# Kernel optimization log

Measured on AMD Instinct MI355X. Metric: run time of the kernel, lower is better.

## Reference

```python
import jax, jax.numpy as jnp
import numpy as np

B, C, H, W, P = 16, 512, 64, 64, 32


def setup_inputs() -> dict:
    key = jax.random.key(0)
    k1, k2, k3 = jax.random.split(key, 3)
    inputs = jax.random.normal(k1, (B, C, H, W), dtype=jnp.float32)
    weight = jax.random.uniform(k2, (P, C, 1, 1), dtype=jnp.float32)
    smooth_factor = jax.random.normal(k3, (P,), dtype=jnp.float32)
    return {"inputs": inputs, "weight": weight, "smooth_factor": smooth_factor}


def reference(inputs, weight, smooth_factor):
    b, c, h, w = inputs.shape
    p = weight.shape[0]
    n = h * w
    centers = weight.reshape(p, c)                      # [P,C]
    x = inputs.reshape(b, c, n)                         # [B,C,N]

    # distance-based logits: 2<c,x> - |x|^2 - |c|^2, clamped at 0
    cx = jnp.einsum('pc,bcn->bpn', centers, x)          # [B,P,N]
    x_sq = jnp.sum(x * x, axis=1, keepdims=True)        # [B,1,N]
    c_sq = jnp.sum(centers * centers, axis=1)[None, :, None]  # [1,P,1]
    beta = jax.nn.sigmoid(smooth_factor)                # [P]
    logits = jnp.minimum(2.0 * cx - x_sq - c_sq, 0.0) / beta[None, :, None]
    assign = jax.nn.softmax(logits, axis=1)             # [B,P,N]

    # assignment-weighted pooling
    qx = jnp.einsum('bpn,bcn->bpc', assign, x)          # [B,P,C]
    sum_ass = jnp.clip(jnp.sum(assign, axis=2, keepdims=True), 1e-5)  # [B,P,1]
    sigma = jnp.sqrt(beta / 2.0)                        # [P]
    out = (qx / sum_ass - centers[None, :, :]) / sigma[None, :, None]

    # L2-normalize over channel dim (torch F.normalize, eps=1e-12)
    norm = jnp.sqrt(jnp.sum(out * out, axis=2, keepdims=True))
    outputs = out / jnp.maximum(norm, 1e-12)
    outputs_t = jnp.transpose(outputs, (0, 2, 1))       # [B,C,P]
    assign_map = assign.reshape(b, p, h, w)             # [B,P,H,W]
    return outputs_t, assign_map
```

## Files before the change

### kernel.cpp

```cpp
#include <hip/hip_runtime.h>

constexpr int BB = 16;
constexpr int CC = 512;
constexpr int PP = 32;
constexpr int NN = 4096;

using f32x4 = __attribute__((ext_vector_type(4))) float;
using bf16x8 = __attribute__((ext_vector_type(8))) short;
typedef unsigned int uint;

__device__ __forceinline__ ushort f2bf(float f) {
  unsigned u = __builtin_bit_cast(unsigned, f);
  u += 0x7FFFu + ((u >> 16) & 1u);
  return (ushort)(u >> 16);
}

__global__ __launch_bounds__(64) void prep_kernel(
    const float* __restrict__ w, const float* __restrict__ sf,
    float* __restrict__ beta, float* __restrict__ rbeta,
    float* __restrict__ csq, float* __restrict__ sum_ass,
    ushort* __restrict__ chi, ushort* __restrict__ clo) {
  int p = blockIdx.x;
  int t = threadIdx.x;
  if (t < 16) sum_ass[p * 16 + t] = 0.f;
  float s = 0.f;
  int c8 = t * 8;
  float4 v0 = *(const float4*)&w[p * CC + c8];
  float4 v1 = *(const float4*)&w[p * CC + c8 + 4];
  ushort h[8], l[8];
  float vv[8] = {v0.x, v0.y, v0.z, v0.w, v1.x, v1.y, v1.z, v1.w};
#pragma unroll
  for (int i = 0; i < 8; ++i) {
    s = fmaf(vv[i], vv[i], s);
    h[i] = f2bf(vv[i]);
    float hf = __builtin_bit_cast(float, (uint)h[i] << 16);
    l[i] = f2bf(vv[i] - hf);
  }
  *(ushort4*)&chi[p * CC + c8] = make_ushort4(h[0], h[1], h[2], h[3]);
  *(ushort4*)&chi[p * CC + c8 + 4] = make_ushort4(h[4], h[5], h[6], h[7]);
  *(ushort4*)&clo[p * CC + c8] = make_ushort4(l[0], l[1], l[2], l[3]);
  *(ushort4*)&clo[p * CC + c8 + 4] = make_ushort4(l[4], l[5], l[6], l[7]);
#pragma unroll
  for (int off = 32; off; off >>= 1) s += __shfl_down(s, off);
  if (t == 0) {
    csq[p] = s;
    float e = __expf(-sf[p]);
    rbeta[p] = 1.f + e;
    beta[p] = 1.f / (1.f + e);
  }
}

__global__ __launch_bounds__(256) void assign_kernel(
    const float* __restrict__ x, const ushort* __restrict__ chi,
    const ushort* __restrict__ clo, const float* __restrict__ rbeta_,
    const float* __restrict__ csq_, float* __restrict__ assign_out,
    float* __restrict__ sum_ass) {
  int tid = threadIdx.x;
  int wv = tid >> 6, lane = tid & 63;
  int l15 = lane & 15, lg = lane >> 4;
  int b = blockIdx.x >> 5;
  int n0 = (blockIdx.x & 31) * 128 + wv * 32;

  const float* xb = x + (size_t)b * CC * NN + n0 + l15;

  f32x4 acc[2][2];
#pragma unroll
  for (int i = 0; i < 2; ++i)
#pragma unroll
    for (int j = 0; j < 2; ++j) acc[i][j] = {0.f, 0.f, 0.f, 0.f};
  float xsq[2] = {0.f, 0.f};

#pragma unroll 4
  for (int ks = 0; ks < 16; ++ks) {
    int c0 = ks * 32 + lg * 8;
    bf16x8 Ah0 = *(const bf16x8*)&chi[l15 * CC + c0];
    bf16x8 Ah1 = *(const bf16x8*)&chi[(l15 + 16) * CC + c0];
    bf16x8 Al0 = *(const bf16x8*)&clo[l15 * CC + c0];
    bf16x8 Al1 = *(const bf16x8*)&clo[(l15 + 16) * CC + c0];
#pragma unroll
    for (int nf = 0; nf < 2; ++nf) {
      float xv[8];
#pragma unroll
      for (int j = 0; j < 8; ++j)
        xv[j] = xb[(size_t)(c0 + j) * NN + nf * 16];
      union { bf16x8 v; ushort e[8]; } Bh, Bl;
#pragma unroll
      for (int j = 0; j < 8; ++j) {
        xsq[nf] = fmaf(xv[j], xv[j], xsq[nf]);
        ushort h = f2bf(xv[j]);
        float hf = __builtin_bit_cast(float, (uint)h << 16);
        Bh.e[j] = h;
        Bl.e[j] = f2bf(xv[j] - hf);
      }
      acc[0][nf] = __builtin_amdgcn_mfma_f32_16x16x32_bf16(Ah0, Bh.v, acc[0][nf], 0, 0, 0);
      acc[1][nf] = __builtin_amdgcn_mfma_f32_16x16x32_bf16(Ah1, Bh.v, acc[1][nf], 0, 0, 0);
      acc[0][nf] = __builtin_amdgcn_mfma_f32_16x16x32_bf16(Ah0, Bl.v, acc[0][nf], 0, 0, 0);
      acc[1][nf] = __builtin_amdgcn_mfma_f32_16x16x32_bf16(Ah1, Bl.v, acc[1][nf], 0, 0, 0);
      acc[0][nf] = __builtin_amdgcn_mfma_f32_16x16x32_bf16(Al0, Bh.v, acc[0][nf], 0, 0, 0);
      acc[1][nf] = __builtin_amdgcn_mfma_f32_16x16x32_bf16(Al1, Bh.v, acc[1][nf], 0, 0, 0);
    }
  }

#pragma unroll
  for (int nf = 0; nf < 2; ++nf) {
    xsq[nf] += __shfl_xor(xsq[nf], 16);
    xsq[nf] += __shfl_xor(xsq[nf], 32);
  }

  float csqv[2][4], rbv[2][4];
#pragma unroll
  for (int pf = 0; pf < 2; ++pf)
#pragma unroll
    for (int i = 0; i < 4; ++i) {
      int p = pf * 16 + lg * 4 + i;
      csqv[pf][i] = csq_[p];
      rbv[pf][i] = rbeta_[p];
    }

  float L[2][2][4];
  float m[2] = {-3.4e38f, -3.4e38f};
#pragma unroll
  for (int pf = 0; pf < 2; ++pf)
#pragma unroll
    for (int nf = 0; nf < 2; ++nf)
#pragma unroll
      for (int i = 0; i < 4; ++i) {
        float l = fminf(2.f * acc[pf][nf][i] - xsq[nf] - csqv[pf][i], 0.f) * rbv[pf][i];
        L[pf][nf][i] = l;
        m[nf] = fmaxf(m[nf], l);
      }
#pragma unroll
  for (int nf = 0; nf < 2; ++nf) {
    m[nf] = fmaxf(m[nf], __shfl_xor(m[nf], 16));
    m[nf] = fmaxf(m[nf], __shfl_xor(m[nf], 32));
  }
  float s[2] = {0.f, 0.f};
#pragma unroll
  for (int pf = 0; pf < 2; ++pf)
#pragma unroll
    for (int nf = 0; nf < 2; ++nf)
#pragma unroll
      for (int i = 0; i < 4; ++i) {
        float e = __expf(L[pf][nf][i] - m[nf]);
        L[pf][nf][i] = e;
        s[nf] += e;
      }
#pragma unroll
  for (int nf = 0; nf < 2; ++nf) {
    s[nf] += __shfl_xor(s[nf], 16);
    s[nf] += __shfl_xor(s[nf], 32);
    s[nf] = 1.f / s[nf];
  }

  float* aoB = assign_out + (size_t)b * PP * NN + n0 + l15;
#pragma unroll
  for (int pf = 0; pf < 2; ++pf)
#pragma unroll
    for (int i = 0; i < 4; ++i) {
      int p = pf * 16 + lg * 4 + i;
      float a0 = L[pf][0][i] * s[0];
      float a1 = L[pf][1][i] * s[1];
      aoB[(size_t)p * NN] = a0;
      aoB[(size_t)p * NN + 16] = a1;
      float v = a0 + a1;
      v += __shfl_xor(v, 1); v += __shfl_xor(v, 2);
      v += __shfl_xor(v, 4); v += __shfl_xor(v, 8);
      if (l15 == 0) atomicAdd(&sum_ass[b * PP + p], v);
    }
}

__global__ __launch_bounds__(256) void qx_kernel(
    const float* __restrict__ x, const float* __restrict__ assign,
    float* __restrict__ qx_part) {
  __shared__ ushort xbf[128][136];
  __shared__ ushort abf[32][136];

  int tid = threadIdx.x;
  int b = blockIdx.y;
  int kc = blockIdx.x >> 2;
  int ct = blockIdx.x & 3;
  int wv = tid >> 6, lane = tid & 63;
  int l15 = lane & 15, lg = lane >> 4;

  const float* xb = x + ((size_t)b * CC + ct * 128) * NN + kc * 512;
  const float* ab = assign + (size_t)b * PP * NN + kc * 512;

  int c_s = tid >> 1;
  int nh  = (tid & 1) << 6;
  int p_s = tid >> 3;
  int na  = (tid & 7) << 4;

  f32x4 acc[2][2];
#pragma unroll
  for (int i = 0; i < 2; ++i)
#pragma unroll
    for (int j = 0; j < 2; ++j) acc[i][j] = {0.f, 0.f, 0.f, 0.f};

  for (int ch = 0; ch < 4; ++ch) {
    int nb = ch * 128;
    if (ch) __syncthreads();
#pragma unroll
    for (int h = 0; h < 2; ++h) {
      float4 v[8];
#pragma unroll
      for (int i = 0; i < 8; ++i)
        v[i] = *(const float4*)&xb[(size_t)c_s * NN + nb + nh + h * 32 + i * 4];
#pragma unroll
      for (int i = 0; i < 8; ++i) {
        ushort4 u;
        u.x = f2bf(v[i].x); u.y = f2bf(v[i].y);
        u.z = f2bf(v[i].z); u.w = f2bf(v[i].w);
        *(ushort4*)&xbf[c_s][nh + h * 32 + i * 4] = u;
      }
    }
    {
      float4 v[4];
#pragma unroll
      for (int i = 0; i < 4; ++i)
        v[i] = *(const float4*)&ab[(size_t)p_s * NN + nb + na + i * 4];
#pragma unroll
      for (int i = 0; i < 4; ++i) {
        ushort4 u;
        u.x = f2bf(v[i].x); u.y = f2bf(v[i].y);
        u.z = f2bf(v[i].z); u.w = f2bf(v[i].w);
        *(ushort4*)&abf[p_s][na + i * 4] = u;
      }
    }
    __syncthreads();
#pragma unroll
    for (int ks = 0; ks < 4; ++ks) {
      int nf = ks * 32 + lg * 8;
      bf16x8 a0 = *(const bf16x8*)&abf[l15][nf];
      bf16x8 a1 = *(const bf16x8*)&abf[16 + l15][nf];
      bf16x8 b0 = *(const bf16x8*)&xbf[wv * 32 + l15][nf];
      bf16x8 b1 = *(const bf16x8*)&xbf[wv * 32 + 16 + l15][nf];
      acc[0][0] = __builtin_amdgcn_mfma_f32_16x16x32_bf16(a0, b0, acc[0][0], 0, 0, 0);
      acc[0][1] = __builtin_amdgcn_mfma_f32_16x16x32_bf16(a0, b1, acc[0][1], 0, 0, 0);
      acc[1][0] = __builtin_amdgcn_mfma_f32_16x16x32_bf16(a1, b0, acc[1][0], 0, 0, 0);
      acc[1][1] = __builtin_amdgcn_mfma_f32_16x16x32_bf16(a1, b1, acc[1][1], 0, 0, 0);
    }
  }

#pragma unroll
  for (int pf = 0; pf < 2; ++pf)
#pragma unroll
    for (int cf = 0; cf < 2; ++cf)
#pragma unroll
      for (int i = 0; i < 4; ++i) {
        int p = pf * 16 + lg * 4 + i;
        int c = ct * 128 + wv * 32 + cf * 16 + l15;
        qx_part[(((size_t)kc * BB + b) * PP + p) * CC + c] = acc[pf][cf][i];
      }
}

__global__ __launch_bounds__(256) void finalize_kernel(
    const float* __restrict__ qx_part, const float* __restrict__ w,
    const float* __restrict__ beta, const float* __restrict__ sum_ass,
    float* __restrict__ out_t) {
  int b = blockIdx.x >> 5;
  int p = blockIdx.x & 31;
  int tid = threadIdx.x;
  int wave = tid >> 6, lane = tid & 63;

  float inv_sa = 1.f / fmaxf(sum_ass[b * PP + p], 1e-5f);
  float rsig = rsqrtf(0.5f * beta[p]);

  int c0 = tid, c1 = tid + 256;
  float q0 = 0.f, q1 = 0.f;
#pragma unroll
  for (int kc = 0; kc < 8; ++kc) {
    const float* row = qx_part + (((size_t)kc * BB + b) * PP + p) * CC;
    q0 += row[c0];
    q1 += row[c1];
  }
  const float* wrow = w + (size_t)p * CC;
  float t0 = (q0 * inv_sa - wrow[c0]) * rsig;
  float t1 = (q1 * inv_sa - wrow[c1]) * rsig;

  float nr = t0 * t0 + t1 * t1;
#pragma unroll
  for (int off = 32; off; off >>= 1) nr += __shfl_down(nr, off);
  __shared__ float red[4];
  if (lane == 0) red[wave] = nr;
  __syncthreads();
  float norm2 = red[0] + red[1] + red[2] + red[3];
  float scale = 1.f / fmaxf(sqrtf(norm2), 1e-12f);

  float* ob = out_t + (size_t)b * CC * PP + p;
  ob[(size_t)c0 * PP] = t0 * scale;
  ob[(size_t)c1 * PP] = t1 * scale;
}

extern "C" void kernel_launch(void* const* d_in, const int* in_sizes, int n_in,
                              void* d_out, int out_size, void* d_ws,
                              size_t ws_size, hipStream_t stream) {
  const float* x = (const float*)d_in[0];
  const float* w = (const float*)d_in[1];
  const float* sf = (const float*)d_in[2];

  float* out_t = (float*)d_out;
  float* assign = out_t + (size_t)BB * CC * PP;

  float* ws = (float*)d_ws;
  float* beta = ws;
  float* rbeta = ws + 32;
  float* csq = ws + 64;
  float* sum_ass = ws + 96;
  float* qx_part = ws + 608;
  ushort* chi = (ushort*)(ws + 608 + 2097152);
  ushort* clo = chi + PP * CC;

  prep_kernel<<<PP, 64, 0, stream>>>(w, sf, beta, rbeta, csq, sum_ass,
                                     chi, clo);
  assign_kernel<<<512, 256, 0, stream>>>(x, chi, clo, rbeta, csq, assign,
                                         sum_ass);
  qx_kernel<<<dim3(32, BB), 256, 0, stream>>>(x, assign, qx_part);
  finalize_kernel<<<BB * PP, 256, 0, stream>>>(qx_part, w, beta, sum_ass,
                                               out_t);
}
```

Baseline: 85.66 us.

## Drop LDS staging in qx kernel, write bf16 assign, and atomically accumulate qx

The assign kernel now gives each wave 16 columns instead of 32, doubling the grid, and also writes a bf16 copy of the assignments for the second GEMM. The qx kernel drops shared-memory staging: each wave loads bf16 assign and fp32 x straight from global memory, converts x to bf16 in registers, and accumulates its partial result into qx with atomics. This removes the fp32 partial buffer and the reduction loop in finalize, and prep now zeroes the combined sum_ass and qx region. In exchange it adds many float atomics and relies on uncoalesced per-lane global loads without LDS reuse.

New measurement: 125.0 us. 1.46x slower.

```diff
diff --git a/kernel.cpp b/kernel.cpp
--- a/kernel.cpp
+++ b/kernel.cpp
@@ -18,11 +18,14 @@
 __global__ __launch_bounds__(64) void prep_kernel(
     const float* __restrict__ w, const float* __restrict__ sf,
     float* __restrict__ beta, float* __restrict__ rbeta,
-    float* __restrict__ csq, float* __restrict__ sum_ass,
+    float* __restrict__ csq, float* __restrict__ zbase,
     ushort* __restrict__ chi, ushort* __restrict__ clo) {
+  int t = threadIdx.x;
+  float4* z4 = (float4*)zbase;
+  for (int i = blockIdx.x * 64 + t; i < 65664; i += 32 * 64)
+    z4[i] = make_float4(0.f, 0.f, 0.f, 0.f);
+
   int p = blockIdx.x;
-  int t = threadIdx.x;
-  if (t < 16) sum_ass[p * 16 + t] = 0.f;
   float s = 0.f;
   int c8 = t * 8;
   float4 v0 = *(const float4*)&w[p * CC + c8];
@@ -50,25 +53,23 @@
   }
 }
 
-__global__ __launch_bounds__(256) void assign_kernel(
+__global__ __launch_bounds__(256, 4) void assign_kernel(
     const float* __restrict__ x, const ushort* __restrict__ chi,
     const ushort* __restrict__ clo, const float* __restrict__ rbeta_,
     const float* __restrict__ csq_, float* __restrict__ assign_out,
-    float* __restrict__ sum_ass) {
+    ushort* __restrict__ abf16, float* __restrict__ sum_ass) {
   int tid = threadIdx.x;
   int wv = tid >> 6, lane = tid & 63;
   int l15 = lane & 15, lg = lane >> 4;
-  int b = blockIdx.x >> 5;
-  int n0 = (blockIdx.x & 31) * 128 + wv * 32;
+  int b = blockIdx.x >> 6;
+  int n0 = (blockIdx.x & 63) * 64 + wv * 16;
 
   const float* xb = x + (size_t)b * CC * NN + n0 + l15;
 
-  f32x4 acc[2][2];
-#pragma unroll
-  for (int i = 0; i < 2; ++i)
-#pragma unroll
-    for (int j = 0; j < 2; ++j) acc[i][j] = {0.f, 0.f, 0.f, 0.f};
-  float xsq[2] = {0.f, 0.f};
+  f32x4 acc[2];
+  acc[0] = {0.f, 0.f, 0.f, 0.f};
+  acc[1] = {0.f, 0.f, 0.f, 0.f};
+  float xsq = 0.f;
 
 #pragma unroll 4
   for (int ks = 0; ks < 16; ++ks) {
@@ -77,35 +78,28 @@
     bf16x8 Ah1 = *(const bf16x8*)&chi[(l15 + 16) * CC + c0];
     bf16x8 Al0 = *(const bf16x8*)&clo[l15 * CC + c0];
     bf16x8 Al1 = *(const bf16x8*)&clo[(l15 + 16) * CC + c0];
-#pragma unroll
-    for (int nf = 0; nf < 2; ++nf) {
-      float xv[8];
-#pragma unroll
-      for (int j = 0; j < 8; ++j)
-        xv[j] = xb[(size_t)(c0 + j) * NN + nf * 16];
-      union { bf16x8 v; ushort e[8]; } Bh, Bl;
-#pragma unroll
-      for (int j = 0; j < 8; ++j) {
-        xsq[nf] = fmaf(xv[j], xv[j], xsq[nf]);
-        ushort h = f2bf(xv[j]);
-        float hf = __builtin_bit_cast(float, (uint)h << 16);
-        Bh.e[j] = h;
-        Bl.e[j] = f2bf(xv[j] - hf);
-      }
-      acc[0][nf] = __builtin_amdgcn_mfma_f32_16x16x32_bf16(Ah0, Bh.v, acc[0][nf], 0, 0, 0);
-      acc[1][nf] = __builtin_amdgcn_mfma_f32_16x16x32_bf16(Ah1, Bh.v, acc[1][nf], 0, 0, 0);
-      acc[0][nf] = __builtin_amdgcn_mfma_f32_16x16x32_bf16(Ah0, Bl.v, acc[0][nf], 0, 0, 0);
-      acc[1][nf] = __builtin_amdgcn_mfma_f32_16x16x32_bf16(Ah1, Bl.v, acc[1][nf], 0, 0, 0);
-      acc[0][nf] = __builtin_amdgcn_mfma_f32_16x16x32_bf16(Al0, Bh.v, acc[0][nf], 0, 0, 0);
-      acc[1][nf] = __builtin_amdgcn_mfma_f32_16x16x32_bf16(Al1, Bh.v, acc[1][nf], 0, 0, 0);
-    }
-  }
-
-#pragma unroll
-  for (int nf = 0; nf < 2; ++nf) {
-    xsq[nf] += __shfl_xor(xsq[nf], 16);
-    xsq[nf] += __shfl_xor(xsq[nf], 32);
-  }
+    float xv[8];
+#pragma unroll
+    for (int j = 0; j < 8; ++j) xv[j] = xb[(size_t)(c0 + j) * NN];
+    union { bf16x8 v; ushort e[8]; } Bh, Bl;
+#pragma unroll
+    for (int j = 0; j < 8; ++j) {
+      xsq = fmaf(xv[j], xv[j], xsq);
+      ushort h = f2bf(xv[j]);
+      float hf = __builtin_bit_cast(float, (uint)h << 16);
+      Bh.e[j] = h;
+      Bl.e[j] = f2bf(xv[j] - hf);
+    }
+    acc[0] = __builtin_amdgcn_mfma_f32_16x16x32_bf16(Ah0, Bh.v, acc[0], 0, 0, 0);
+    acc[1] = __builtin_amdgcn_mfma_f32_16x16x32_bf16(Ah1, Bh.v, acc[1], 0, 0, 0);
+    acc[0] = __builtin_amdgcn_mfma_f32_16x16x32_bf16(Ah0, Bl.v, acc[0], 0, 0, 0);
+    acc[1] = __builtin_amdgcn_mfma_f32_16x16x32_bf16(Ah1, Bl.v, acc[1], 0, 0, 0);
+    acc[0] = __builtin_amdgcn_mfma_f32_16x16x32_bf16(Al0, Bh.v, acc[0], 0, 0, 0);
+    acc[1] = __builtin_amdgcn_mfma_f32_16x16x32_bf16(Al1, Bh.v, acc[1], 0, 0, 0);
+  }
+
+  xsq += __shfl_xor(xsq, 16);
+  xsq += __shfl_xor(xsq, 32);
 
   float csqv[2][4], rbv[2][4];
 #pragma unroll
@@ -117,127 +111,84 @@
       rbv[pf][i] = rbeta_[p];
     }
 
-  float L[2][2][4];
-  float m[2] = {-3.4e38f, -3.4e38f};
-#pragma unroll
-  for (int pf = 0; pf < 2; ++pf)
-#pragma unroll
-    for (int nf = 0; nf < 2; ++nf)
-#pragma unroll
-      for (int i = 0; i < 4; ++i) {
-        float l = fminf(2.f * acc[pf][nf][i] - xsq[nf] - csqv[pf][i], 0.f) * rbv[pf][i];
-        L[pf][nf][i] = l;
-        m[nf] = fmaxf(m[nf], l);
-      }
-#pragma unroll
-  for (int nf = 0; nf < 2; ++nf) {
-    m[nf] = fmaxf(m[nf], __shfl_xor(m[nf], 16));
-    m[nf] = fmaxf(m[nf], __shfl_xor(m[nf], 32));
-  }
-  float s[2] = {0.f, 0.f};
-#pragma unroll
-  for (int pf = 0; pf < 2; ++pf)
-#pragma unroll
-    for (int nf = 0; nf < 2; ++nf)
-#pragma unroll
-      for (int i = 0; i < 4; ++i) {
-        float e = __expf(L[pf][nf][i] - m[nf]);
-        L[pf][nf][i] = e;
-        s[nf] += e;
-      }
-#pragma unroll
-  for (int nf = 0; nf < 2; ++nf) {
-    s[nf] += __shfl_xor(s[nf], 16);
-    s[nf] += __shfl_xor(s[nf], 32);
-    s[nf] = 1.f / s[nf];
-  }
+  float L[2][4];
+  float m = -3.4e38f;
+#pragma unroll
+  for (int pf = 0; pf < 2; ++pf)
+#pragma unroll
+    for (int i = 0; i < 4; ++i) {
+      float l = fminf(2.f * acc[pf][i] - xsq - csqv[pf][i], 0.f) * rbv[pf][i];
+      L[pf][i] = l;
+      m = fmaxf(m, l);
+    }
+  m = fmaxf(m, __shfl_xor(m, 16));
+  m = fmaxf(m, __shfl_xor(m, 32));
+  float s = 0.f;
+#pragma unroll
+  for (int pf = 0; pf < 2; ++pf)
+#pragma unroll
+    for (int i = 0; i < 4; ++i) {
+      float e = __expf(L[pf][i] - m);
+      L[pf][i] = e;
+      s += e;
+    }
+  s += __shfl_xor(s, 16);
+  s += __shfl_xor(s, 32);
+  float inv = 1.f / s;
 
   float* aoB = assign_out + (size_t)b * PP * NN + n0 + l15;
+  ushort* abB = abf16 + (size_t)b * PP * NN + n0 + l15;
 #pragma unroll
   for (int pf = 0; pf < 2; ++pf)
 #pragma unroll
     for (int i = 0; i < 4; ++i) {
       int p = pf * 16 + lg * 4 + i;
-      float a0 = L[pf][0][i] * s[0];
-      float a1 = L[pf][1][i] * s[1];
-      aoB[(size_t)p * NN] = a0;
-      aoB[(size_t)p * NN + 16] = a1;
-      float v = a0 + a1;
+      float a = L[pf][i] * inv;
+      aoB[(size_t)p * NN] = a;
+      abB[(size_t)p * NN] = f2bf(a);
+      float v = a;
       v += __shfl_xor(v, 1); v += __shfl_xor(v, 2);
       v += __shfl_xor(v, 4); v += __shfl_xor(v, 8);
       if (l15 == 0) atomicAdd(&sum_ass[b * PP + p], v);
     }
 }
 
-__global__ __launch_bounds__(256) void qx_kernel(
-    const float* __restrict__ x, const float* __restrict__ assign,
-    float* __restrict__ qx_part) {
-  __shared__ ushort xbf[128][136];
-  __shared__ ushort abf[32][136];
-
+__global__ __launch_bounds__(256, 4) void qx_kernel(
+    const float* __restrict__ x, const ushort* __restrict__ abf16,
+    float* __restrict__ qx) {
   int tid = threadIdx.x;
-  int b = blockIdx.y;
-  int kc = blockIdx.x >> 2;
-  int ct = blockIdx.x & 3;
   int wv = tid >> 6, lane = tid & 63;
   int l15 = lane & 15, lg = lane >> 4;
-
-  const float* xb = x + ((size_t)b * CC + ct * 128) * NN + kc * 512;
-  const float* ab = assign + (size_t)b * PP * NN + kc * 512;
-
-  int c_s = tid >> 1;
-  int nh  = (tid & 1) << 6;
-  int p_s = tid >> 3;
-  int na  = (tid & 7) << 4;
-
-  f32x4 acc[2][2];
+  int b = blockIdx.y;
+  int ct = blockIdx.x >> 2;
+  int kc = (blockIdx.x & 3) * 4 + wv;
+
+  const ushort* ab = abf16 + (size_t)b * PP * NN + kc * 256;
+  const float* xb = x + ((size_t)b * CC + ct * 32) * NN + kc * 256;
+
+  f32x4 q[2][2];
 #pragma unroll
   for (int i = 0; i < 2; ++i)
 #pragma unroll
-    for (int j = 0; j < 2; ++j) acc[i][j] = {0.f, 0.f, 0.f, 0.f};
-
-  for (int ch = 0; ch < 4; ++ch) {
-    int nb = ch * 128;
-    if (ch) __syncthreads();
-#pragma unroll
-    for (int h = 0; h < 2; ++h) {
-      float4 v[8];
-#pragma unroll
-      for (int i = 0; i < 8; ++i)
-        v[i] = *(const float4*)&xb[(size_t)c_s * NN + nb + nh + h * 32 + i * 4];
-#pragma unroll
-      for (int i = 0; i < 8; ++i) {
-        ushort4 u;
-        u.x = f2bf(v[i].x); u.y = f2bf(v[i].y);
-        u.z = f2bf(v[i].z); u.w = f2bf(v[i].w);
-        *(ushort4*)&xbf[c_s][nh + h * 32 + i * 4] = u;
-      }
-    }
-    {
-      float4 v[4];
-#pragma unroll
-      for (int i = 0; i < 4; ++i)
-        v[i] = *(const float4*)&ab[(size_t)p_s * NN + nb + na + i * 4];
-#pragma unroll
-      for (int i = 0; i < 4; ++i) {
-        ushort4 u;
-        u.x = f2bf(v[i].x); u.y = f2bf(v[i].y);
-        u.z = f2bf(v[i].z); u.w = f2bf(v[i].w);
-        *(ushort4*)&abf[p_s][na + i * 4] = u;
-      }
-    }
-    __syncthreads();
-#pragma unroll
-    for (int ks = 0; ks < 4; ++ks) {
-      int nf = ks * 32 + lg * 8;
-      bf16x8 a0 = *(const bf16x8*)&abf[l15][nf];
-      bf16x8 a1 = *(const bf16x8*)&abf[16 + l15][nf];
-      bf16x8 b0 = *(const bf16x8*)&xbf[wv * 32 + l15][nf];
-      bf16x8 b1 = *(const bf16x8*)&xbf[wv * 32 + 16 + l15][nf];
-      acc[0][0] = __builtin_amdgcn_mfma_f32_16x16x32_bf16(a0, b0, acc[0][0], 0, 0, 0);
-      acc[0][1] = __builtin_amdgcn_mfma_f32_16x16x32_bf16(a0, b1, acc[0][1], 0, 0, 0);
-      acc[1][0] = __builtin_amdgcn_mfma_f32_16x16x32_bf16(a1, b0, acc[1][0], 0, 0, 0);
-      acc[1][1] = __builtin_amdgcn_mfma_f32_16x16x32_bf16(a1, b1, acc[1][1], 0, 0, 0);
+    for (int j = 0; j < 2; ++j) q[i][j] = {0.f, 0.f, 0.f, 0.f};
+
+#pragma unroll 2
+  for (int ks = 0; ks < 8; ++ks) {
+    int ko = ks * 32 + lg * 8;
+    bf16x8 A0 = *(const bf16x8*)&ab[(size_t)l15 * NN + ko];
+    bf16x8 A1 = *(const bf16x8*)&ab[(size_t)(l15 + 16) * NN + ko];
+#pragma unroll
+    for (int cf = 0; cf < 2; ++cf) {
+      const float* xr = &xb[(size_t)(cf * 16 + l15) * NN + ko];
+      float4 u0 = *(const float4*)xr;
+      float4 u1 = *(const float4*)(xr + 4);
+      union { bf16x8 v; ushort e[8]; } Bv;
+      Bv.e[0] = f2bf(u0.x); Bv.e[1] = f2bf(u0.y);
+      Bv.e[2] = f2bf(u0.z); Bv.e[3] = f2bf(u0.w);
+      Bv.e[4] = f2bf(u1.x); Bv.e[5] = f2bf(u1.y);
+      Bv.e[6] = f2bf(u1.z); Bv.e[7] = f2bf(u1.w);
+      q[0][cf] = __builtin_amdgcn_mfma_f32_16x16x32_bf16(A0, Bv.v, q[0][cf], 0, 0, 0);
+      q[1][cf] = __builtin_amdgcn_mfma_f32_16x16x32_bf16(A1, Bv.v, q[1][cf], 0, 0, 0);
     }
   }
 
@@ -248,13 +199,13 @@
 #pragma unroll
       for (int i = 0; i < 4; ++i) {
         int p = pf * 16 + lg * 4 + i;
-        int c = ct * 128 + wv * 32 + cf * 16 + l15;
-        qx_part[(((size_t)kc * BB + b) * PP + p) * CC + c] = acc[pf][cf][i];
+        int c = ct * 32 + cf * 16 + l15;
+        atomicAdd(&qx[((size_t)b * PP + p) * CC + c], q[pf][cf][i]);
       }
 }
 
 __global__ __launch_bounds__(256) void finalize_kernel(
-    const float* __restrict__ qx_part, const float* __restrict__ w,
+    const float* __restrict__ qx, const float* __restrict__ w,
     const float* __restrict__ beta, const float* __restrict__ sum_ass,
     float* __restrict__ out_t) {
   int b = blockIdx.x >> 5;
@@ -266,16 +217,10 @@
   float rsig = rsqrtf(0.5f * beta[p]);
 
   int c0 = tid, c1 = tid + 256;
-  float q0 = 0.f, q1 = 0.f;
-#pragma unroll
-  for (int kc = 0; kc < 8; ++kc) {
-    const float* row = qx_part + (((size_t)kc * BB + b) * PP + p) * CC;
-    q0 += row[c0];
-    q1 += row[c1];
-  }
+  const float* qrow = qx + ((size_t)b * PP + p) * CC;
   const float* wrow = w + (size_t)p * CC;
-  float t0 = (q0 * inv_sa - wrow[c0]) * rsig;
-  float t1 = (q1 * inv_sa - wrow[c1]) * rsig;
+  float t0 = (qrow[c0] * inv_sa - wrow[c0]) * rsig;
+  float t1 = (qrow[c1] * inv_sa - wrow[c1]) * rsig;
 
   float nr = t0 * t0 + t1 * t1;
 #pragma unroll
@@ -306,15 +251,15 @@
   float* rbeta = ws + 32;
   float* csq = ws + 64;
   float* sum_ass = ws + 96;
-  float* qx_part = ws + 608;
-  ushort* chi = (ushort*)(ws + 608 + 2097152);
+  float* qx = ws + 608;
+  ushort* chi = (ushort*)(ws + 608 + 262144);
   ushort* clo = chi + PP * CC;
+  ushort* abf16 = clo + PP * CC;
 
   prep_kernel<<<PP, 64, 0, stream>>>(w, sf, beta, rbeta, csq, sum_ass,
                                      chi, clo);
-  assign_kernel<<<512, 256, 0, stream>>>(x, chi, clo, rbeta, csq, assign,
-                                         sum_ass);
-  qx_kernel<<<dim3(32, BB), 256, 0, stream>>>(x, assign, qx_part);
-  finalize_kernel<<<BB * PP, 256, 0, stream>>>(qx_part, w, beta, sum_ass,
-                                               out_t);
-}
+  assign_kernel<<<BB * 64, 256, 0, stream>>>(x, chi, clo, rbeta, csq,
+                                             assign, abf16, sum_ass);
+  qx_kernel<<<dim3(64, BB), 256, 0, stream>>>(x, abf16, qx);
+  finalize_kernel<<<BB * PP, 256, 0, stream>>>(qx, w, beta, sum_ass, out_t);
+}
```

## Split assign kernel channel reduction across wave pairs with LDS combine

Applied to the files above, without the earlier changes.

The assign kernel now splits the 512-channel reduction between two waves per 32-column tile. Each wave processes half the channels, and the partial accumulators and x^2 sums are combined through shared memory. The grid doubles to 1024 blocks, each covering 64 columns, and the launch bounds now request 4 blocks per CU to raise parallelism and hide latency on the strided x loads. The cost is an LDS round-trip and a block barrier, and half the waves sit idle during the epilogue.

Result: slower. 89.48 us (+4.5%).

```diff
diff --git a/kernel.cpp b/kernel.cpp
--- a/kernel.cpp
+++ b/kernel.cpp
@@ -50,16 +50,19 @@
   }
 }
 
-__global__ __launch_bounds__(256) void assign_kernel(
+__global__ __launch_bounds__(256, 4) void assign_kernel(
     const float* __restrict__ x, const ushort* __restrict__ chi,
     const ushort* __restrict__ clo, const float* __restrict__ rbeta_,
     const float* __restrict__ csq_, float* __restrict__ assign_out,
     float* __restrict__ sum_ass) {
+  __shared__ float red[2][64][18];
+
   int tid = threadIdx.x;
   int wv = tid >> 6, lane = tid & 63;
   int l15 = lane & 15, lg = lane >> 4;
-  int b = blockIdx.x >> 5;
-  int n0 = (blockIdx.x & 31) * 128 + wv * 32;
+  int ns = wv & 1, ch = wv >> 1;
+  int b = blockIdx.x >> 6;
+  int n0 = (blockIdx.x & 63) * 64 + ns * 32;
 
   const float* xb = x + (size_t)b * CC * NN + n0 + l15;
 
@@ -71,8 +74,8 @@
   float xsq[2] = {0.f, 0.f};
 
 #pragma unroll 4
-  for (int ks = 0; ks < 16; ++ks) {
-    int c0 = ks * 32 + lg * 8;
+  for (int ks = 0; ks < 8; ++ks) {
+    int c0 = ch * 256 + ks * 32 + lg * 8;
     bf16x8 Ah0 = *(const bf16x8*)&chi[l15 * CC + c0];
     bf16x8 Ah1 = *(const bf16x8*)&chi[(l15 + 16) * CC + c0];
     bf16x8 Al0 = *(const bf16x8*)&clo[l15 * CC + c0];
@@ -99,6 +102,28 @@
       acc[0][nf] = __builtin_amdgcn_mfma_f32_16x16x32_bf16(Al0, Bh.v, acc[0][nf], 0, 0, 0);
       acc[1][nf] = __builtin_amdgcn_mfma_f32_16x16x32_bf16(Al1, Bh.v, acc[1][nf], 0, 0, 0);
     }
+  }
+
+  if (ch == 1) {
+    float* r = &red[ns][lane][0];
+    *(f32x4*)&r[0] = acc[0][0];
+    *(f32x4*)&r[4] = acc[0][1];
+    *(f32x4*)&r[8] = acc[1][0];
+    *(f32x4*)&r[12] = acc[1][1];
+    r[16] = xsq[0];
+    r[17] = xsq[1];
+  }
+  __syncthreads();
+  if (ch == 1) return;
+
+  {
+    const float* r = &red[ns][lane][0];
+    acc[0][0] += *(const f32x4*)&r[0];
+    acc[0][1] += *(const f32x4*)&r[4];
+    acc[1][0] += *(const f32x4*)&r[8];
+    acc[1][1] += *(const f32x4*)&r[12];
+    xsq[0] += r[16];
+    xsq[1] += r[17];
   }
 
 #pragma unroll
@@ -312,8 +337,8 @@
 
   prep_kernel<<<PP, 64, 0, stream>>>(w, sf, beta, rbeta, csq, sum_ass,
                                      chi, clo);
-  assign_kernel<<<512, 256, 0, stream>>>(x, chi, clo, rbeta, csq, assign,
-                                         sum_ass);
+  assign_kernel<<<BB * 64, 256, 0, stream>>>(x, chi, clo, rbeta, csq,
+                                             assign, sum_ass);
   qx_kernel<<<dim3(32, BB), 256, 0, stream>>>(x, assign, qx_part);
   finalize_kernel<<<BB * PP, 256, 0, stream>>>(qx_part, w, beta, sum_ass,
                                                out_t);
```

## Drop LDS staging in qx GEMM, use per-wave split-K with atomics

Applied to the files above, without the earlier changes.

Each wave of the qx kernel now loads assign and x fragments straight from global memory into registers and converts them to bf16 for the MFMAs, with no shared-memory staging or block barriers. The reduction dimension is split 16 ways across waves, and partial sums are combined with atomicAdd into a single qx buffer. That buffer and sum_ass are zeroed in prep_kernel, and finalize_kernel no longer sums the partial buffers. The aim is to remove LDS traffic, barriers and the large partial-result write and re-read. In exchange, the assign tile is re-read once for each of 16 channel tiles instead of 4, global loads are row-strided, and 16-way atomic contention is added.

New measurement: 93.07 us. 1.09x slower.

```diff
diff --git a/kernel.cpp b/kernel.cpp
--- a/kernel.cpp
+++ b/kernel.cpp
@@ -18,11 +18,14 @@
 __global__ __launch_bounds__(64) void prep_kernel(
     const float* __restrict__ w, const float* __restrict__ sf,
     float* __restrict__ beta, float* __restrict__ rbeta,
-    float* __restrict__ csq, float* __restrict__ sum_ass,
+    float* __restrict__ csq, float* __restrict__ zbase,
     ushort* __restrict__ chi, ushort* __restrict__ clo) {
   int p = blockIdx.x;
   int t = threadIdx.x;
-  if (t < 16) sum_ass[p * 16 + t] = 0.f;
+  float4* z4 = (float4*)zbase;
+  for (int i = blockIdx.x * 64 + t; i < 65664; i += 32 * 64)
+    z4[i] = make_float4(0.f, 0.f, 0.f, 0.f);
+
   float s = 0.f;
   int c8 = t * 8;
   float4 v0 = *(const float4*)&w[p * CC + c8];
@@ -169,75 +172,57 @@
     }
 }
 
-__global__ __launch_bounds__(256) void qx_kernel(
+__global__ __launch_bounds__(256, 4) void qx_kernel(
     const float* __restrict__ x, const float* __restrict__ assign,
-    float* __restrict__ qx_part) {
-  __shared__ ushort xbf[128][136];
-  __shared__ ushort abf[32][136];
-
+    float* __restrict__ qx) {
   int tid = threadIdx.x;
-  int b = blockIdx.y;
-  int kc = blockIdx.x >> 2;
-  int ct = blockIdx.x & 3;
   int wv = tid >> 6, lane = tid & 63;
   int l15 = lane & 15, lg = lane >> 4;
-
-  const float* xb = x + ((size_t)b * CC + ct * 128) * NN + kc * 512;
-  const float* ab = assign + (size_t)b * PP * NN + kc * 512;
-
-  int c_s = tid >> 1;
-  int nh  = (tid & 1) << 6;
-  int p_s = tid >> 3;
-  int na  = (tid & 7) << 4;
-
-  f32x4 acc[2][2];
+  int b = blockIdx.y;
+  int ct = blockIdx.x >> 2;
+  int kc = (blockIdx.x & 3) * 4 + wv;
+
+  const float* ab = assign + (size_t)b * PP * NN + kc * 256;
+  const float* xb = x + ((size_t)b * CC + ct * 32) * NN + kc * 256;
+
+  f32x4 q[2][2];
 #pragma unroll
   for (int i = 0; i < 2; ++i)
 #pragma unroll
-    for (int j = 0; j < 2; ++j) acc[i][j] = {0.f, 0.f, 0.f, 0.f};
-
-  for (int ch = 0; ch < 4; ++ch) {
-    int nb = ch * 128;
-    if (ch) __syncthreads();
-#pragma unroll
-    for (int h = 0; h < 2; ++h) {
-      float4 v[8];
-#pragma unroll
-      for (int i = 0; i < 8; ++i)
-        v[i] = *(const float4*)&xb[(size_t)c_s * NN + nb + nh + h * 32 + i * 4];
-#pragma unroll
-      for (int i = 0; i < 8; ++i) {
-        ushort4 u;
-        u.x = f2bf(v[i].x); u.y = f2bf(v[i].y);
-        u.z = f2bf(v[i].z); u.w = f2bf(v[i].w);
-        *(ushort4*)&xbf[c_s][nh + h * 32 + i * 4] = u;
-      }
-    }
+    for (int j = 0; j < 2; ++j) q[i][j] = {0.f, 0.f, 0.f, 0.f};
+
+#pragma unroll 2
+  for (int ks = 0; ks < 8; ++ks) {
+    int ko = ks * 32 + lg * 8;
+    union { bf16x8 v; ushort e[8]; } A0, A1;
     {
-      float4 v[4];
-#pragma unroll
-      for (int i = 0; i < 4; ++i)
-        v[i] = *(const float4*)&ab[(size_t)p_s * NN + nb + na + i * 4];
-#pragma unroll
-      for (int i = 0; i < 4; ++i) {
-        ushort4 u;
-        u.x = f2bf(v[i].x); u.y = f2bf(v[i].y);
-        u.z = f2bf(v[i].z); u.w = f2bf(v[i].w);
-        *(ushort4*)&abf[p_s][na + i * 4] = u;
-      }
-    }
-    __syncthreads();
-#pragma unroll
-    for (int ks = 0; ks < 4; ++ks) {
-      int nf = ks * 32 + lg * 8;
-      bf16x8 a0 = *(const bf16x8*)&abf[l15][nf];
-      bf16x8 a1 = *(const bf16x8*)&abf[16 + l15][nf];
-      bf16x8 b0 = *(const bf16x8*)&xbf[wv * 32 + l15][nf];
-      bf16x8 b1 = *(const bf16x8*)&xbf[wv * 32 + 16 + l15][nf];
-      acc[0][0] = __builtin_amdgcn_mfma_f32_16x16x32_bf16(a0, b0, acc[0][0], 0, 0, 0);
-      acc[0][1] = __builtin_amdgcn_mfma_f32_16x16x32_bf16(a0, b1, acc[0][1], 0, 0, 0);
-      acc[1][0] = __builtin_amdgcn_mfma_f32_16x16x32_bf16(a1, b0, acc[1][0], 0, 0, 0);
-      acc[1][1] = __builtin_amdgcn_mfma_f32_16x16x32_bf16(a1, b1, acc[1][1], 0, 0, 0);
+      const float* ar = &ab[(size_t)l15 * NN + ko];
+      float4 u0 = *(const float4*)ar;
+      float4 u1 = *(const float4*)(ar + 4);
+      A0.e[0] = f2bf(u0.x); A0.e[1] = f2bf(u0.y);
+      A0.e[2] = f2bf(u0.z); A0.e[3] = f2bf(u0.w);
+      A0.e[4] = f2bf(u1.x); A0.e[5] = f2bf(u1.y);
+      A0.e[6] = f2bf(u1.z); A0.e[7] = f2bf(u1.w);
+      const float* ar1 = &ab[(size_t)(l15 + 16) * NN + ko];
+      float4 w0 = *(const float4*)ar1;
+      float4 w1 = *(const float4*)(ar1 + 4);
+      A1.e[0] = f2bf(w0.x); A1.e[1] = f2bf(w0.y);
+      A1.e[2] = f2bf(w0.z); A1.e[3] = f2bf(w0.w);
+      A1.e[4] = f2bf(w1.x); A1.e[5] = f2bf(w1.y);
+      A1.e[6] = f2bf(w1.z); A1.e[7] = f2bf(w1.w);
+    }
+#pragma unroll
+    for (int cf = 0; cf < 2; ++cf) {
+      const float* xr = &xb[(size_t)(cf * 16 + l15) * NN + ko];
+      float4 u0 = *(const float4*)xr;
+      float4 u1 = *(const float4*)(xr + 4);
+      union { bf16x8 v; ushort e[8]; } Bv;
+      Bv.e[0] = f2bf(u0.x); Bv.e[1] = f2bf(u0.y);
+      Bv.e[2] = f2bf(u0.z); Bv.e[3] = f2bf(u0.w);
+      Bv.e[4] = f2bf(u1.x); Bv.e[5] = f2bf(u1.y);
+      Bv.e[6] = f2bf(u1.z); Bv.e[7] = f2bf(u1.w);
+      q[0][cf] = __builtin_amdgcn_mfma_f32_16x16x32_bf16(A0.v, Bv.v, q[0][cf], 0, 0, 0);
+      q[1][cf] = __builtin_amdgcn_mfma_f32_16x16x32_bf16(A1.v, Bv.v, q[1][cf], 0, 0, 0);
     }
   }
 
@@ -248,13 +233,13 @@
 #pragma unroll
       for (int i = 0; i < 4; ++i) {
         int p = pf * 16 + lg * 4 + i;
-        int c = ct * 128 + wv * 32 + cf * 16 + l15;
-        qx_part[(((size_t)kc * BB + b) * PP + p) * CC + c] = acc[pf][cf][i];
+        int c = ct * 32 + cf * 16 + l15;
+        atomicAdd(&qx[((size_t)b * PP + p) * CC + c], q[pf][cf][i]);
       }
 }
 
 __global__ __launch_bounds__(256) void finalize_kernel(
-    const float* __restrict__ qx_part, const float* __restrict__ w,
+    const float* __restrict__ qx, const float* __restrict__ w,
     const float* __restrict__ beta, const float* __restrict__ sum_ass,
     float* __restrict__ out_t) {
   int b = blockIdx.x >> 5;
@@ -266,16 +251,10 @@
   float rsig = rsqrtf(0.5f * beta[p]);
 
   int c0 = tid, c1 = tid + 256;
-  float q0 = 0.f, q1 = 0.f;
-#pragma unroll
-  for (int kc = 0; kc < 8; ++kc) {
-    const float* row = qx_part + (((size_t)kc * BB + b) * PP + p) * CC;
-    q0 += row[c0];
-    q1 += row[c1];
-  }
+  const float* qrow = qx + ((size_t)b * PP + p) * CC;
   const float* wrow = w + (size_t)p * CC;
-  float t0 = (q0 * inv_sa - wrow[c0]) * rsig;
-  float t1 = (q1 * inv_sa - wrow[c1]) * rsig;
+  float t0 = (qrow[c0] * inv_sa - wrow[c0]) * rsig;
+  float t1 = (qrow[c1] * inv_sa - wrow[c1]) * rsig;
 
   float nr = t0 * t0 + t1 * t1;
 #pragma unroll
@@ -306,15 +285,14 @@
   float* rbeta = ws + 32;
   float* csq = ws + 64;
   float* sum_ass = ws + 96;
-  float* qx_part = ws + 608;
-  ushort* chi = (ushort*)(ws + 608 + 2097152);
+  float* qx = ws + 608;
+  ushort* chi = (ushort*)(ws + 608 + 262144);
   ushort* clo = chi + PP * CC;
 
   prep_kernel<<<PP, 64, 0, stream>>>(w, sf, beta, rbeta, csq, sum_ass,
                                      chi, clo);
   assign_kernel<<<512, 256, 0, stream>>>(x, chi, clo, rbeta, csq, assign,
                                          sum_ass);
-  qx_kernel<<<dim3(32, BB), 256, 0, stream>>>(x, assign, qx_part);
-  finalize_kernel<<<BB * PP, 256, 0, stream>>>(qx_part, w, beta, sum_ass,
-                                               out_t);
-}
+  qx_kernel<<<dim3(64, BB), 256, 0, stream>>>(x, assign, qx);
+  finalize_kernel<<<BB * PP, 256, 0, stream>>>(qx, w, beta, sum_ass, out_t);
+}
```
